# Kernel optimization log

Hardware: AMD Instinct MI355X
Metric: run time of the kernel (lower is better)

Reference implementation:

```python
import jax, jax.numpy as jnp
import numpy as np

MAX_SEGMENTS = 196
MAX_PIX = 400        # max_pixels_per_segment
C = 3                # n_channels
EMBED = 768


def setup_inputs() -> dict:
    key = jax.random.key(0)
    k1, k2, k3, k4 = jax.random.split(key, 4)
    B, H, W = 64, 224, 224
    img = jax.random.normal(k1, (B, C, H, W), jnp.float32)
    segments = jax.random.randint(k2, (B, H, W), 0, MAX_SEGMENTS).astype(jnp.int32)
    fan_in = C * MAX_PIX
    Wp = jax.random.normal(k3, (EMBED, fan_in), jnp.float32) / np.sqrt(fan_in)
    b = jax.random.normal(k4, (EMBED,), jnp.float32) * 0.01
    return {"img": img, "segments": segments, "W": Wp, "b": b}


def _gather_pad(img_flat, seg_flat):
    # img_flat: [C, P], seg_flat: [P] int32. Builds [S, C*MAX_PIX] padded buffer.
    P = seg_flat.shape[0]
    order = jnp.argsort(seg_flat, stable=True)          # stable -> keeps scan order (matches torch truncation)
    s = seg_flat[order]                                  # sorted segment ids, [P]
    counts = jnp.zeros((MAX_SEGMENTS,), jnp.int32).at[seg_flat].add(1)
    starts = jnp.concatenate([jnp.zeros((1,), jnp.int32),
                              jnp.cumsum(counts)[:-1].astype(jnp.int32)])
    rank = jnp.arange(P, dtype=jnp.int32) - starts[s]    # within-segment position
    valid = rank < MAX_PIX                               # truncate overly large segments
    rank_c = jnp.where(valid, rank, 0)
    vals = jnp.where(valid[:, None], img_flat.T[order], 0.0)  # [P, C]
    buf = jnp.zeros((MAX_SEGMENTS, C, MAX_PIX), img_flat.dtype)
    buf = buf.at[s, :, rank_c].add(vals)                 # invalid rows add zeros -> no-op
    # torch does pixels_in_segment.flatten() on (C, MAX_PIX) -> channel-major layout
    return buf.reshape(MAX_SEGMENTS, C * MAX_PIX)


def reference(img, segments, W, b):
    B = img.shape[0]
    img_flat = img.reshape(B, C, -1)          # [B, C, H*W]
    seg_flat = segments.reshape(B, -1)        # [B, H*W]
    feats = jax.vmap(_gather_pad)(img_flat, seg_flat)   # [B, S, C*MAX_PIX]
    return jnp.einsum('bsf,ef->bse', feats, W) + b      # nn.Linear
```

## Files before the change

### kernel.cpp

```cpp
#include <hip/hip_runtime.h>
#include <hip/hip_bf16.h>

#define B_      64
#define C_      3
#define H_      224
#define W_      224
#define P_      (H_*W_)
#define S_      196
#define MAXPIX  400
#define E_      768
#define K_      1200
#define KP_     1216
#define CHUNK_  512
#define NCH_    (P_/CHUNK_)
#define M_      (B_*S_)

#define RANK_BLOCKS  (B_*NCH_)
#define WCONV_BLOCKS ((E_*KP_)/512)
#define PREFIX_BLOCKS (B_*S_)
#define ZERO_BLOCKS  2048
#define FEATS_BYTES_ ((size_t)M_ * KP_ * 2)


typedef __attribute__((ext_vector_type(8))) short short8;
typedef __attribute__((ext_vector_type(4))) float f32x4;

__device__ inline unsigned short f2bf(float f) {
  union { float f; unsigned int u; } x; x.f = f;
  return (unsigned short)((x.u + 0x7fffu + ((x.u >> 16) & 1u)) >> 16);
}

__device__ inline int xcd_chunk(int wg, int nwg) {
  int q = nwg >> 3;
  return (wg & 7) * q + (wg >> 3);
}

__global__ __launch_bounds__(512) void prep_k(const float* __restrict__ Wf,
                                              unsigned short* __restrict__ Wb,
                                              const int* __restrict__ seg,
                                              int* __restrict__ hist,
                                              unsigned short* __restrict__ rloc) {
  int blk = blockIdx.x;
  if (blk >= RANK_BLOCKS) {
    int idx = (blk - RANK_BLOCKS) * 512 + threadIdx.x;
    int e = idx / KP_, k = idx - e * KP_;
    float v = 0.f;
    if (k < K_) {
      int r = k / 3, c = k - r * 3;
      v = Wf[e * K_ + c * MAXPIX + r];
    }
    Wb[idx] = f2bf(v);
    return;
  }
  int b = blk / NCH_, ch = blk % NCH_;
  int tid = threadIdx.x, wave = tid >> 6, lane = tid & 63;
  int p = ch * CHUNK_ + tid;
  int s = seg[b * P_ + p];

  __shared__ int lhist[8][S_];
  for (int i = tid; i < 8 * S_; i += 512) ((int*)lhist)[i] = 0;
  __syncthreads();

  int r = 0;
  #pragma unroll 1
  for (int j = 0; j < 64; ++j) {
    int sj = __shfl(s, j);
    r += (j < lane && sj == s) ? 1 : 0;
  }
  atomicAdd(&lhist[wave][s], 1);
  __syncthreads();

  int off = 0;
  for (int w2 = 0; w2 < wave; ++w2) off += lhist[w2][s];
  rloc[b * P_ + p] = (unsigned short)(off + r);

  if (tid < S_) {
    int t = 0;
    #pragma unroll
    for (int w2 = 0; w2 < 8; ++w2) t += lhist[w2][tid];
    hist[(b * NCH_ + ch) * S_ + tid] = t;
  }
}

__global__ __launch_bounds__(128) void prefix_zero_k(int* __restrict__ hist,
                                                     int4* __restrict__ feats4) {
  int blk = blockIdx.x;
  if (blk >= PREFIX_BLOCKS) {
    int j = blk - PREFIX_BLOCKS;
    int r = j & 7;
    const int REG4 = (int)(FEATS_BYTES_ / 8 / 16);
    int4* base = feats4 + (size_t)r * REG4;
    int4 z = make_int4(0, 0, 0, 0);
    for (int i = (j >> 3) * 128 + threadIdx.x; i < REG4; i += (ZERO_BLOCKS / 8) * 128)
      base[i] = z;
    return;
  }
  int b = blk / S_, s = blk % S_;
  int t = threadIdx.x;
  __shared__ int sc[128];
  int v = (t < NCH_) ? hist[(b * NCH_ + t) * S_ + s] : 0;
  sc[t] = v;
  __syncthreads();
  #pragma unroll
  for (int off = 1; off < 128; off <<= 1) {
    int x = (t >= off) ? sc[t - off] : 0;
    __syncthreads();
    sc[t] += x;
    __syncthreads();
  }
  if (t < NCH_) hist[(b * NCH_ + t) * S_ + s] = sc[t] - v;
}

__global__ __launch_bounds__(256) void scatter_vals_k(const float* __restrict__ img,
                                                      const int* __restrict__ seg,
                                                      const int* __restrict__ starts,
                                                      const unsigned short* __restrict__ rloc,
                                                      unsigned short* __restrict__ feats) {
  int wg = xcd_chunk(blockIdx.x, B_ * (P_ / 256));
  int b = wg / (P_ / 256);
  int p = (wg % (P_ / 256)) * 256 + threadIdx.x;
  int s = seg[b * P_ + p];
  int rank = starts[(b * NCH_ + (p >> 9)) * S_ + s] + rloc[b * P_ + p];
  if (rank < MAXPIX) {
    const float* ib = img + (size_t)b * C_ * P_;
    unsigned short c0 = f2bf(ib[p]);
    unsigned short c1 = f2bf(ib[P_ + p]);
    unsigned short c2 = f2bf(ib[2 * P_ + p]);
    char* bp = (char*)(feats + (size_t)(b * S_ + s) * KP_) + 6 * (size_t)rank;
    if (rank & 1) {
      *(unsigned short*)bp = c0;
      *(unsigned int*)(bp + 2) = (unsigned int)c1 | ((unsigned int)c2 << 16);
    } else {
      *(unsigned int*)bp = (unsigned int)c0 | ((unsigned int)c1 << 16);
      *(unsigned short*)(bp + 4) = c2;
    }
  }
}

__global__ __launch_bounds__(256) void gemm_k(const unsigned short* __restrict__ A,
                                              const unsigned short* __restrict__ Bw,
                                              const float* __restrict__ bias,
                                              float* __restrict__ out) {
  int bid;
  {
    int wg = blockIdx.x, q = 588 / 8, r = 588 % 8;
    int xcd = wg % 8, idx = wg / 8;
    bid = (xcd < r) ? xcd * (q + 1) + idx : r * (q + 1) + (xcd - r) * q + idx;
  }
  const int nb = bid % (E_ / 128);
  const int mb = bid / (E_ / 128);
  const int tid = threadIdx.x;
  const int w = tid >> 6, l = tid & 63;
  const int wr = w >> 1, wc = w & 1;

  __shared__ __align__(16) unsigned short As[128 * 32];
  __shared__ __align__(16) unsigned short Bs[128 * 32];

  f32x4 acc[4][4] = {};

  const int lrow = l >> 2;
  const int lcol = (l & 3) * 8;
  const int kk = (l >> 4) * 8;

  for (int k0 = 0; k0 < KP_; k0 += 32) {
    #pragma unroll
    for (int q = 0; q < 2; ++q) {
      int r = (w * 2 + q) * 16 + lrow;
      const unsigned short* ga = A + (size_t)(mb * 128 + r) * KP_ + k0 + lcol;
      __builtin_amdgcn_global_load_lds((const __attribute__((address_space(1))) unsigned int*)ga,
                                       (__attribute__((address_space(3))) unsigned int*)&As[(w * 2 + q) * 512],
                                       16, 0, 0);
      const unsigned short* gb = Bw + (size_t)(nb * 128 + r) * KP_ + k0 + lcol;
      __builtin_amdgcn_global_load_lds((const __attribute__((address_space(1))) unsigned int*)gb,
                                       (__attribute__((address_space(3))) unsigned int*)&Bs[(w * 2 + q) * 512],
                                       16, 0, 0);
    }
    __syncthreads();

    short8 af[4], bf[4];
    #pragma unroll
    for (int mi = 0; mi < 4; ++mi)
      af[mi] = *(const short8*)&As[(wr * 64 + mi * 16 + (l & 15)) * 32 + kk];
    #pragma unroll
    for (int ni = 0; ni < 4; ++ni)
      bf[ni] = *(const short8*)&Bs[(wc * 64 + ni * 16 + (l & 15)) * 32 + kk];
    #pragma unroll
    for (int mi = 0; mi < 4; ++mi)
      #pragma unroll
      for (int ni = 0; ni < 4; ++ni)
        acc[mi][ni] = __builtin_amdgcn_mfma_f32_16x16x32_bf16(af[mi], bf[ni], acc[mi][ni], 0, 0, 0);
    __syncthreads();
  }

  const int r0 = (l >> 4) * 4;
  const int c0 = l & 15;
  #pragma unroll
  for (int mi = 0; mi < 4; ++mi) {
    #pragma unroll
    for (int ni = 0; ni < 4; ++ni) {
      int col = nb * 128 + wc * 64 + ni * 16 + c0;
      float bv = bias[col];
      int row = mb * 128 + wr * 64 + mi * 16 + r0;
      #pragma unroll
      for (int r = 0; r < 4; ++r)
        out[(size_t)(row + r) * E_ + col] = acc[mi][ni][r] + bv;
    }
  }
}

extern "C" void kernel_launch(void* const* d_in, const int* in_sizes, int n_in,
                              void* d_out, int out_size, void* d_ws, size_t ws_size,
                              hipStream_t stream) {
  const float* img  = (const float*)d_in[0];
  const int*   seg  = (const int*)d_in[1];
  const float* Wf   = (const float*)d_in[2];
  const float* bias = (const float*)d_in[3];
  float* out = (float*)d_out;

  constexpr size_t WB_BYTES    = (size_t)E_ * KP_ * 2;
  constexpr size_t RLOC_BYTES  = (size_t)B_ * P_ * 2;
  char* ws = (char*)d_ws;
  unsigned short* Wb    = (unsigned short*)ws;
  unsigned short* feats = (unsigned short*)(ws + WB_BYTES);
  unsigned short* rloc  = (unsigned short*)(ws + WB_BYTES + FEATS_BYTES_);
  int*            hist  = (int*)(ws + WB_BYTES + FEATS_BYTES_ + RLOC_BYTES);

  prep_k<<<RANK_BLOCKS + WCONV_BLOCKS, 512, 0, stream>>>(Wf, Wb, seg, hist, rloc);
  prefix_zero_k<<<PREFIX_BLOCKS + ZERO_BLOCKS, 128, 0, stream>>>(hist, (int4*)feats);
  scatter_vals_k<<<B_ * (P_ / 256), 256, 0, stream>>>(img, seg, hist, rloc, feats);
  gemm_k<<<(M_ / 128) * (E_ / 128), 256, 0, stream>>>(feats, Wb, bias, out);
}
```

Measured before the change: 229.9 us.

## Pad feature pixels to 4 channels and zero only unfilled tails

Changes the packed feature layout from 3 bf16 per pixel (K padded to 1216) to 4 bf16 per pixel (K=1600), so each scatter is one aligned 8-byte store, and permutes the weights to match. The full-buffer zeroing pass is replaced by per-row tail zeroing driven by segment counts taken from the prefix scan, and is merged into the scatter kernel. Scratch buffers move into the output allocation. In exchange the GEMM does about 32% more K work and reads a larger feature matrix.

After: 222.4 us. 1.03x faster.

```diff
diff --git a/kernel.cpp b/kernel.cpp
--- a/kernel.cpp
+++ b/kernel.cpp
@@ -10,16 +10,16 @@
 #define MAXPIX  400
 #define E_      768
 #define K_      1200
-#define KP_     1216
+#define KP2_    1600
 #define CHUNK_  512
 #define NCH_    (P_/CHUNK_)
 #define M_      (B_*S_)
 
 #define RANK_BLOCKS  (B_*NCH_)
-#define WCONV_BLOCKS ((E_*KP_)/512)
+#define WCONV_BLOCKS ((E_*KP2_)/512)
 #define PREFIX_BLOCKS (B_*S_)
-#define ZERO_BLOCKS  2048
-#define FEATS_BYTES_ ((size_t)M_ * KP_ * 2)
+#define SCAT_BLOCKS  (B_*(P_/256))
+#define TAIL_BLOCKS  (M_/16)
 
 
 typedef __attribute__((ext_vector_type(8))) short short8;
@@ -43,12 +43,9 @@
   int blk = blockIdx.x;
   if (blk >= RANK_BLOCKS) {
     int idx = (blk - RANK_BLOCKS) * 512 + threadIdx.x;
-    int e = idx / KP_, k = idx - e * KP_;
-    float v = 0.f;
-    if (k < K_) {
-      int r = k / 3, c = k - r * 3;
-      v = Wf[e * K_ + c * MAXPIX + r];
-    }
+    int e = idx / KP2_, k = idx - e * KP2_;
+    int r = k >> 2, c = k & 3;
+    float v = (c < 3) ? Wf[e * K_ + c * MAXPIX + r] : 0.f;
     Wb[idx] = f2bf(v);
     return;
   }
@@ -82,20 +79,8 @@
   }
 }
 
-__global__ __launch_bounds__(128) void prefix_zero_k(int* __restrict__ hist,
-                                                     int4* __restrict__ feats4) {
-  int blk = blockIdx.x;
-  if (blk >= PREFIX_BLOCKS) {
-    int j = blk - PREFIX_BLOCKS;
-    int r = j & 7;
-    const int REG4 = (int)(FEATS_BYTES_ / 8 / 16);
-    int4* base = feats4 + (size_t)r * REG4;
-    int4 z = make_int4(0, 0, 0, 0);
-    for (int i = (j >> 3) * 128 + threadIdx.x; i < REG4; i += (ZERO_BLOCKS / 8) * 128)
-      base[i] = z;
-    return;
-  }
-  int b = blk / S_, s = blk % S_;
+__global__ __launch_bounds__(128) void prefix_k(int* __restrict__ hist, int* __restrict__ cnts) {
+  int b = blockIdx.x / S_, s = blockIdx.x % S_;
   int t = threadIdx.x;
   __shared__ int sc[128];
   int v = (t < NCH_) ? hist[(b * NCH_ + t) * S_ + s] : 0;
@@ -109,31 +94,42 @@
     __syncthreads();
   }
   if (t < NCH_) hist[(b * NCH_ + t) * S_ + s] = sc[t] - v;
-}
-
-__global__ __launch_bounds__(256) void scatter_vals_k(const float* __restrict__ img,
+  if (t == NCH_ - 1) {
+    int tot = sc[t];
+    cnts[b * S_ + s] = tot < MAXPIX ? tot : MAXPIX;
+  }
+}
+
+__global__ __launch_bounds__(256) void scatter_tail_k(const float* __restrict__ img,
                                                       const int* __restrict__ seg,
                                                       const int* __restrict__ starts,
                                                       const unsigned short* __restrict__ rloc,
+                                                      const int* __restrict__ cnts,
                                                       unsigned short* __restrict__ feats) {
-  int wg = xcd_chunk(blockIdx.x, B_ * (P_ / 256));
+  int wg = xcd_chunk(blockIdx.x, SCAT_BLOCKS + TAIL_BLOCKS);
+  if (wg >= SCAT_BLOCKS) {
+    int t0 = wg - SCAT_BLOCKS;
+    int row = t0 * 16 + (threadIdx.x >> 4);
+    int l16 = threadIdx.x & 15;
+    int cnt = cnts[row];
+    unsigned short* frow = feats + (size_t)row * KP2_;
+    ushort4 z = make_ushort4(0, 0, 0, 0);
+    for (int r = cnt + l16; r < MAXPIX; r += 16)
+      *(ushort4*)&frow[r * 4] = z;
+    return;
+  }
   int b = wg / (P_ / 256);
   int p = (wg % (P_ / 256)) * 256 + threadIdx.x;
   int s = seg[b * P_ + p];
   int rank = starts[(b * NCH_ + (p >> 9)) * S_ + s] + rloc[b * P_ + p];
   if (rank < MAXPIX) {
     const float* ib = img + (size_t)b * C_ * P_;
-    unsigned short c0 = f2bf(ib[p]);
-    unsigned short c1 = f2bf(ib[P_ + p]);
-    unsigned short c2 = f2bf(ib[2 * P_ + p]);
-    char* bp = (char*)(feats + (size_t)(b * S_ + s) * KP_) + 6 * (size_t)rank;
-    if (rank & 1) {
-      *(unsigned short*)bp = c0;
-      *(unsigned int*)(bp + 2) = (unsigned int)c1 | ((unsigned int)c2 << 16);
-    } else {
-      *(unsigned int*)bp = (unsigned int)c0 | ((unsigned int)c1 << 16);
-      *(unsigned short*)(bp + 4) = c2;
-    }
+    ushort4 o;
+    o.x = f2bf(ib[p]);
+    o.y = f2bf(ib[P_ + p]);
+    o.z = f2bf(ib[2 * P_ + p]);
+    o.w = 0;
+    *(ushort4*)&feats[(size_t)(b * S_ + s) * KP2_ + rank * 4] = o;
   }
 }
 
@@ -162,15 +158,15 @@
   const int lcol = (l & 3) * 8;
   const int kk = (l >> 4) * 8;
 
-  for (int k0 = 0; k0 < KP_; k0 += 32) {
+  for (int k0 = 0; k0 < KP2_; k0 += 32) {
     #pragma unroll
     for (int q = 0; q < 2; ++q) {
       int r = (w * 2 + q) * 16 + lrow;
-      const unsigned short* ga = A + (size_t)(mb * 128 + r) * KP_ + k0 + lcol;
+      const unsigned short* ga = A + (size_t)(mb * 128 + r) * KP2_ + k0 + lcol;
       __builtin_amdgcn_global_load_lds((const __attribute__((address_space(1))) unsigned int*)ga,
                                        (__attribute__((address_space(3))) unsigned int*)&As[(w * 2 + q) * 512],
                                        16, 0, 0);
-      const unsigned short* gb = Bw + (size_t)(nb * 128 + r) * KP_ + k0 + lcol;
+      const unsigned short* gb = Bw + (size_t)(nb * 128 + r) * KP2_ + k0 + lcol;
       __builtin_amdgcn_global_load_lds((const __attribute__((address_space(1))) unsigned int*)gb,
                                        (__attribute__((address_space(3))) unsigned int*)&Bs[(w * 2 + q) * 512],
                                        16, 0, 0);
@@ -217,16 +213,19 @@
   const float* bias = (const float*)d_in[3];
   float* out = (float*)d_out;
 
-  constexpr size_t WB_BYTES    = (size_t)E_ * KP_ * 2;
+  constexpr size_t WB_BYTES    = (size_t)E_ * KP2_ * 2;
   constexpr size_t RLOC_BYTES  = (size_t)B_ * P_ * 2;
+  constexpr size_t HIST_BYTES  = (size_t)B_ * NCH_ * S_ * 4;
   char* ws = (char*)d_ws;
   unsigned short* Wb    = (unsigned short*)ws;
   unsigned short* feats = (unsigned short*)(ws + WB_BYTES);
-  unsigned short* rloc  = (unsigned short*)(ws + WB_BYTES + FEATS_BYTES_);
-  int*            hist  = (int*)(ws + WB_BYTES + FEATS_BYTES_ + RLOC_BYTES);
+  char* oscr = (char*)d_out;
+  unsigned short* rloc  = (unsigned short*)oscr;
+  int*            hist  = (int*)(oscr + RLOC_BYTES);
+  int*            cnts  = (int*)(oscr + RLOC_BYTES + HIST_BYTES);
 
   prep_k<<<RANK_BLOCKS + WCONV_BLOCKS, 512, 0, stream>>>(Wf, Wb, seg, hist, rloc);
-  prefix_zero_k<<<PREFIX_BLOCKS + ZERO_BLOCKS, 128, 0, stream>>>(hist, (int4*)feats);
-  scatter_vals_k<<<B_ * (P_ / 256), 256, 0, stream>>>(img, seg, hist, rloc, feats);
+  prefix_k<<<PREFIX_BLOCKS, 128, 0, stream>>>(hist, cnts);
+  scatter_tail_k<<<SCAT_BLOCKS + TAIL_BLOCKS, 256, 0, stream>>>(img, seg, hist, rloc, cnts, feats);
   gemm_k<<<(M_ / 128) * (E_ / 128), 256, 0, stream>>>(feats, Wb, bias, out);
 }
```
